# Kernel tuning notes

Hardware: AMD Instinct MI355X
Metric: run time of the kernel (lower is better)

Reference implementation:

```python
import jax, jax.numpy as jnp
import numpy as np

B, N, C = 4, 2048, 768
H = 12
D = C // H  # head_dim = 64
SCALE = D ** -0.5


def setup_inputs() -> dict:
    key = jax.random.key(0)
    ks = jax.random.split(key, 9)
    x = jax.random.normal(ks[0], (B, N, C), dtype=jnp.float32)
    k_in = jax.random.normal(ks[1], (B, N, C), dtype=jnp.float32)
    v_in = jax.random.normal(ks[2], (B, N, C), dtype=jnp.float32)
    rel_pos_bias = jax.random.normal(ks[3], (H, N, N), dtype=jnp.float32)
    # learned params (nn.Linear stores weight [out, in]; y = x @ W.T + b)
    s = C ** -0.5
    Wq = jax.random.normal(ks[4], (C, C), dtype=jnp.float32) * s
    Wk = jax.random.normal(ks[5], (C, C), dtype=jnp.float32) * s
    Wv = jax.random.normal(ks[6], (C, C), dtype=jnp.float32) * s
    Wp = jax.random.normal(ks[7], (C, C), dtype=jnp.float32) * s
    bp = jax.random.normal(ks[8], (C,), dtype=jnp.float32) * 0.01
    return {"x": x, "k_in": k_in, "v_in": v_in, "rel_pos_bias": rel_pos_bias,
            "Wq": Wq, "Wk": Wk, "Wv": Wv, "Wp": Wp, "bp": bp}


def reference(x, k_in, v_in, rel_pos_bias, Wq, Wk, Wv, Wp, bp):
    # linear projections (no q/k/v bias since qkv_bias=False)
    q = jnp.einsum('bnc,dc->bnd', x, Wq)      # [B,N,C]
    k = jnp.einsum('bnc,dc->bnd', k_in, Wk)   # [B,Nk,C]
    v = jnp.einsum('bnc,dc->bnd', v_in, Wv)   # [B,Nv,C]
    # split heads -> [B,H,N,D]
    q = q.reshape(B, N, H, D).transpose(0, 2, 1, 3) * SCALE
    k = k.reshape(B, -1, H, D).transpose(0, 2, 1, 3)
    v = v.reshape(B, -1, H, D).transpose(0, 2, 1, 3)
    attn = jnp.einsum('bhnd,bhmd->bhnm', q, k)          # [B,H,N,Nk]
    attn = attn + rel_pos_bias[None]                    # additive rel-pos bias
    attn = jax.nn.softmax(attn, axis=-1)
    out = jnp.einsum('bhnm,bhmd->bhnd', attn, v)        # [B,H,N,D]
    out = out.transpose(0, 2, 1, 3).reshape(B, N, C)
    return jnp.einsum('bnc,dc->bnd', out, Wp) + bp
```

## Files before the change

kernel.cpp:

```cpp
#include <hip/hip_runtime.h>
#include <stdint.h>
#include <stddef.h>

#define B_ 4
#define N_ 2048
#define C_ 768
#define H_ 12
#define M_ (B_ * N_)

typedef __attribute__((ext_vector_type(8))) short bf16x8_t;
typedef __attribute__((ext_vector_type(4))) float f32x4_t;

__device__ __forceinline__ unsigned pack2_bf16(float f0, float f1) {
  unsigned u0 = __builtin_bit_cast(unsigned, f0) + 0x8000u;
  unsigned u1 = __builtin_bit_cast(unsigned, f1) + 0x8000u;
  return __builtin_amdgcn_perm(u1, u0, 0x07060302u);
}

__device__ __forceinline__ short f2bf(float f) {
  unsigned u = __builtin_bit_cast(unsigned, f);
  u = (u + 0x7FFFu + ((u >> 16) & 1u)) >> 16;
  return (short)u;
}
__device__ __forceinline__ short f2bf_fast(float f) {
  return (short)((__builtin_bit_cast(unsigned, f) + 0x8000u) >> 16);
}

__device__ __forceinline__ void gload_lds16(const short* g, const short* l) {
  __builtin_amdgcn_global_load_lds(
      (const __attribute__((address_space(1))) void*)g,
      (__attribute__((address_space(3))) void*)l, 16, 0, 0);
}

#define XV 1572864
#define WV 147456
__global__ __launch_bounds__(256) void cvt_all(
    const float* __restrict__ x, const float* __restrict__ kin, const float* __restrict__ vin,
    const float* __restrict__ wq, const float* __restrict__ wk, const float* __restrict__ wv,
    const float* __restrict__ wp,
    unsigned short* __restrict__ xb, unsigned short* __restrict__ kb, unsigned short* __restrict__ vb,
    unsigned short* __restrict__ wqb, unsigned short* __restrict__ wkb, unsigned short* __restrict__ wvb,
    unsigned short* __restrict__ wpb)
{
  int i = blockIdx.x * 256 + threadIdx.x;
  const float* s; unsigned short* d; int off;
  if      (i < XV)            { s = x;   d = xb;  off = i; }
  else if (i < 2 * XV)        { s = kin; d = kb;  off = i - XV; }
  else if (i < 3 * XV)        { s = vin; d = vb;  off = i - 2 * XV; }
  else if (i < 3 * XV + WV)   { s = wq;  d = wqb; off = i - 3 * XV; }
  else if (i < 3 * XV + 2*WV) { s = wk;  d = wkb; off = i - 3 * XV - WV; }
  else if (i < 3 * XV + 3*WV) { s = wv;  d = wvb; off = i - 3 * XV - 2 * WV; }
  else                        { s = wp;  d = wpb; off = i - 3 * XV - 3 * WV; }
  float4 v = ((const float4*)s)[off];
  uint2 p;
  p.x = pack2_bf16(v.x, v.y);
  p.y = pack2_bf16(v.z, v.w);
  ((uint2*)d)[off] = p;
}

__global__ __launch_bounds__(256) void proj_qkv(
    const short* __restrict__ xb, const short* __restrict__ kb, const short* __restrict__ vb,
    const short* __restrict__ wqb, const short* __restrict__ wkb, const short* __restrict__ wvb,
    short* __restrict__ q_ws, short* __restrict__ k_ws, short* __restrict__ vt_ws)
{
  const int z = blockIdx.z;
  const short* A = (z == 0) ? xb : (z == 1) ? kb : vb;
  const short* W = (z == 0) ? wqb : (z == 1) ? wkb : wvb;
  const int m0 = blockIdx.x * 128;
  const int n0 = blockIdx.y * 128;

  __shared__ short As[128 * 64];
  __shared__ short Bs[128 * 64];

  const int t = threadIdx.x;
  const int w = t >> 6, L = t & 63, L15 = L & 15, quad = L >> 4;
  const int wm = w & 1, wn = w >> 1;

  f32x4_t acc[4][4] = {};

  const short* ga = A + (size_t)(m0 + w * 32 + (L >> 3)) * C_ + (L & 7) * 8;
  const short* gb = W + (size_t)(n0 + w * 32 + (L >> 3)) * C_ + (L & 7) * 8;
  const short* la = &As[(w * 32) * 64];
  const short* lb = &Bs[(w * 32) * 64];

  for (int k0 = 0; k0 < C_; k0 += 64) {
    __syncthreads();
    #pragma unroll
    for (int i = 0; i < 4; ++i) {
      gload_lds16(ga + (size_t)i * 8 * C_ + k0, la + i * 512);
      gload_lds16(gb + (size_t)i * 8 * C_ + k0, lb + i * 512);
    }
    __syncthreads();
    #pragma unroll
    for (int kk = 0; kk < 2; ++kk) {
      bf16x8_t af[4], bf[4];
      #pragma unroll
      for (int mt = 0; mt < 4; ++mt)
        af[mt] = *(const bf16x8_t*)&As[(wm * 64 + mt * 16 + L15) * 64 + kk * 32 + quad * 8];
      #pragma unroll
      for (int nt = 0; nt < 4; ++nt)
        bf[nt] = *(const bf16x8_t*)&Bs[(wn * 64 + nt * 16 + L15) * 64 + kk * 32 + quad * 8];
      #pragma unroll
      for (int mt = 0; mt < 4; ++mt)
        #pragma unroll
        for (int nt = 0; nt < 4; ++nt)
          acc[mt][nt] = __builtin_amdgcn_mfma_f32_16x16x32_bf16(af[mt], bf[nt], acc[mt][nt], 0, 0, 0);
    }
  }

  short* outp = (z == 0) ? q_ws : (z == 1) ? k_ws : vt_ws;
  const float mul = (z == 0) ? 0.125f : 1.0f;
  #pragma unroll
  for (int mt = 0; mt < 4; ++mt) {
    const int m_base = m0 + wm * 64 + mt * 16 + quad * 4;
    #pragma unroll
    for (int nt = 0; nt < 4; ++nt) {
      const int c = n0 + wn * 64 + nt * 16 + L15;
      const int h = c >> 6, d = c & 63;
      #pragma unroll
      for (int r = 0; r < 4; ++r) {
        const int m = m_base + r;
        const int b = m >> 11, n = m & 2047;
        const float v = acc[mt][nt][r] * mul;
        size_t idx;
        if (z == 2) idx = ((size_t)(b * H_ + h) * 64 + d) * N_ + n;
        else        idx = ((size_t)(b * H_ + h) * N_ + n) * 64 + d;
        outp[idx] = f2bf(v);
      }
    }
  }
}

__global__ __launch_bounds__(256) void attn(
    const short* __restrict__ q_ws, const short* __restrict__ k_ws,
    const short* __restrict__ vt_ws, const float* __restrict__ rpb,
    short* __restrict__ attn_out)
{
  const int b = blockIdx.x & 3;
  const int m0 = (blockIdx.x >> 2) * 64;
  const int h = blockIdx.y;
  const int bh = b * H_ + h;

  __shared__ short Qs[64][72];
  __shared__ short Ks[64][72];
  __shared__ short Vts[80][72];
  __shared__ short Ps[4][16][72];

  const int t = threadIdx.x;
  const int w = t >> 6, L = t & 63, L15 = L & 15, quad = L >> 4;
  const int sr = t >> 2, sc = (t & 3) << 4;

  const short* qp  = q_ws  + ((size_t)bh * N_ + m0) * 64;
  const short* kp  = k_ws  + (size_t)bh * N_ * 64;
  const short* vtp = vt_ws + (size_t)bh * 64 * N_;
  const float* bpb = rpb + (size_t)h * N_ * N_;

  {
    const short* g = qp + t * 16;
    *(uint4*)&Qs[sr][sc]     = *(const uint4*)g;
    *(uint4*)&Qs[sr][sc + 8] = *(const uint4*)(g + 8);
  }
  for (int i = t; i < 16 * 72; i += 256) {
    const int rr = i / 72, cc = i % 72;
    Vts[64 + rr][cc] = (rr == 0) ? (short)0x3F80 : (short)0;
  }

  f32x4_t o[5] = {};

  for (int kv0 = 0; kv0 < N_; kv0 += 64) {
    __syncthreads();
    {
      const short* gk = kp + (size_t)kv0 * 64 + t * 16;
      *(uint4*)&Ks[sr][sc]     = *(const uint4*)gk;
      *(uint4*)&Ks[sr][sc + 8] = *(const uint4*)(gk + 8);
      const short* gv = vtp + (size_t)sr * N_ + kv0 + sc;
      *(uint4*)&Vts[sr][sc]     = *(const uint4*)gv;
      *(uint4*)&Vts[sr][sc + 8] = *(const uint4*)(gv + 8);
    }
    float bias[4][4];
    {
      const float* bq = bpb + (size_t)(m0 + w * 16 + quad * 4) * N_ + kv0 + L15;
      #pragma unroll
      for (int r = 0; r < 4; ++r)
        #pragma unroll
        for (int nt = 0; nt < 4; ++nt)
          bias[r][nt] = bq[(size_t)r * N_ + nt * 16];
    }
    __syncthreads();

    bf16x8_t a0 = *(const bf16x8_t*)&Qs[w * 16 + L15][quad * 8];
    bf16x8_t a1 = *(const bf16x8_t*)&Qs[w * 16 + L15][32 + quad * 8];
    f32x4_t s[4];
    #pragma unroll
    for (int nt = 0; nt < 4; ++nt) {
      f32x4_t sv = {bias[0][nt], bias[1][nt], bias[2][nt], bias[3][nt]};
      bf16x8_t b0 = *(const bf16x8_t*)&Ks[nt * 16 + L15][quad * 8];
      bf16x8_t b1 = *(const bf16x8_t*)&Ks[nt * 16 + L15][32 + quad * 8];
      sv = __builtin_amdgcn_mfma_f32_16x16x32_bf16(a0, b0, sv, 0, 0, 0);
      s[nt] = __builtin_amdgcn_mfma_f32_16x16x32_bf16(a1, b1, sv, 0, 0, 0);
    }

    #pragma unroll
    for (int nt = 0; nt < 4; ++nt)
      #pragma unroll
      for (int r = 0; r < 4; ++r)
        Ps[w][quad * 4 + r][nt * 16 + L15] = f2bf_fast(__expf(s[nt][r]));

    #pragma unroll
    for (int kk = 0; kk < 2; ++kk) {
      bf16x8_t pa = *(const bf16x8_t*)&Ps[w][L15][kk * 32 + quad * 8];
      #pragma unroll
      for (int nt = 0; nt < 5; ++nt) {
        bf16x8_t vb = *(const bf16x8_t*)&Vts[nt * 16 + L15][kk * 32 + quad * 8];
        o[nt] = __builtin_amdgcn_mfma_f32_16x16x32_bf16(pa, vb, o[nt], 0, 0, 0);
      }
    }
  }

  float rl[4];
  #pragma unroll
  for (int r = 0; r < 4; ++r) {
    const float l = __shfl(o[4][r], quad * 16);
    rl[r] = 1.0f / l;
  }
  const int n_base = m0 + w * 16 + quad * 4;
  #pragma unroll
  for (int nt = 0; nt < 4; ++nt) {
    #pragma unroll
    for (int r = 0; r < 4; ++r) {
      const float v = o[nt][r] * rl[r];
      attn_out[((size_t)(b * N_ + n_base + r)) * C_ + h * 64 + nt * 16 + L15] = f2bf(v);
    }
  }
}

__global__ __launch_bounds__(256) void proj_out(
    const short* __restrict__ Abf, const short* __restrict__ wpb,
    const float* __restrict__ bpv, float* __restrict__ out)
{
  const int m0 = blockIdx.x * 128;
  const int n0 = blockIdx.y * 128;

  __shared__ short As[128 * 64];
  __shared__ short Bs[128 * 64];

  const int t = threadIdx.x;
  const int w = t >> 6, L = t & 63, L15 = L & 15, quad = L >> 4;
  const int wm = w & 1, wn = w >> 1;

  f32x4_t acc[4][4] = {};

  const short* ga = Abf + (size_t)(m0 + w * 32 + (L >> 3)) * C_ + (L & 7) * 8;
  const short* gb = wpb + (size_t)(n0 + w * 32 + (L >> 3)) * C_ + (L & 7) * 8;
  const short* la = &As[(w * 32) * 64];
  const short* lb = &Bs[(w * 32) * 64];

  for (int k0 = 0; k0 < C_; k0 += 64) {
    __syncthreads();
    #pragma unroll
    for (int i = 0; i < 4; ++i) {
      gload_lds16(ga + (size_t)i * 8 * C_ + k0, la + i * 512);
      gload_lds16(gb + (size_t)i * 8 * C_ + k0, lb + i * 512);
    }
    __syncthreads();
    #pragma unroll
    for (int kk = 0; kk < 2; ++kk) {
      bf16x8_t af[4], bf[4];
      #pragma unroll
      for (int mt = 0; mt < 4; ++mt)
        af[mt] = *(const bf16x8_t*)&As[(wm * 64 + mt * 16 + L15) * 64 + kk * 32 + quad * 8];
      #pragma unroll
      for (int nt = 0; nt < 4; ++nt)
        bf[nt] = *(const bf16x8_t*)&Bs[(wn * 64 + nt * 16 + L15) * 64 + kk * 32 + quad * 8];
      #pragma unroll
      for (int mt = 0; mt < 4; ++mt)
        #pragma unroll
        for (int nt = 0; nt < 4; ++nt)
          acc[mt][nt] = __builtin_amdgcn_mfma_f32_16x16x32_bf16(af[mt], bf[nt], acc[mt][nt], 0, 0, 0);
    }
  }

  #pragma unroll
  for (int mt = 0; mt < 4; ++mt) {
    const int m_base = m0 + wm * 64 + mt * 16 + quad * 4;
    #pragma unroll
    for (int nt = 0; nt < 4; ++nt) {
      const int c = n0 + wn * 64 + nt * 16 + L15;
      const float bb = bpv[c];
      #pragma unroll
      for (int r = 0; r < 4; ++r)
        out[(size_t)(m_base + r) * C_ + c] = acc[mt][nt][r] + bb;
    }
  }
}

extern "C" void kernel_launch(void* const* d_in, const int* in_sizes, int n_in,
                              void* d_out, int out_size, void* d_ws, size_t ws_size,
                              hipStream_t stream) {
  const float* x    = (const float*)d_in[0];
  const float* k_in = (const float*)d_in[1];
  const float* v_in = (const float*)d_in[2];
  const float* rpb  = (const float*)d_in[3];
  const float* Wq   = (const float*)d_in[4];
  const float* Wk   = (const float*)d_in[5];
  const float* Wv   = (const float*)d_in[6];
  const float* Wp   = (const float*)d_in[7];
  const float* bp   = (const float*)d_in[8];
  float* out = (float*)d_out;

  const size_t SZ = (size_t)B_ * H_ * N_ * 64 * sizeof(short);
  const size_t WSZ = (size_t)C_ * C_ * sizeof(short);
  char* ws = (char*)d_ws;
  short* q_ws  = (short*)(ws);
  short* k_ws  = (short*)(ws + SZ);
  short* vt_ws = (short*)(ws + 2 * SZ);
  short* ao_ws = (short*)(ws + 3 * SZ);
  short* xb    = (short*)(ws + 4 * SZ);
  short* kb    = (short*)(ws + 5 * SZ);
  short* vb    = (short*)(ws + 6 * SZ);
  short* wqb   = (short*)(ws + 7 * SZ);
  short* wkb   = (short*)(ws + 7 * SZ + WSZ);
  short* wvb   = (short*)(ws + 7 * SZ + 2 * WSZ);
  short* wpb   = (short*)(ws + 7 * SZ + 3 * WSZ);

  cvt_all<<<(3 * XV + 4 * WV + 255) / 256, 256, 0, stream>>>(
      x, k_in, v_in, Wq, Wk, Wv, Wp,
      (unsigned short*)xb, (unsigned short*)kb, (unsigned short*)vb,
      (unsigned short*)wqb, (unsigned short*)wkb, (unsigned short*)wvb, (unsigned short*)wpb);
  proj_qkv<<<dim3(M_ / 128, C_ / 128, 3), 256, 0, stream>>>(
      xb, kb, vb, wqb, wkb, wvb, q_ws, k_ws, vt_ws);
  attn<<<dim3(B_ * (N_ / 64), H_), 256, 0, stream>>>(q_ws, k_ws, vt_ws, rpb, ao_ws);
  proj_out<<<dim3(M_ / 128, C_ / 128), 256, 0, stream>>>(ao_ws, wpb, bp, out);
}
```

Baseline: 512.2 us.

## Stage QKV epilogue through LDS and use direct global-to-LDS loads in attention

The QKV projection epilogue now writes bf16 results into shared memory, transposed for V, and then emits coalesced 16-byte global stores instead of scattered 2-byte stores. The attention kernel replaces register-staged Q/K/V^T loads with gload_lds16 direct-to-LDS copies into unpadded 64-wide tiles. The cost is two extra barriers and a larger LDS footprint in the projection kernel. The unpadded Q/K/V tiles may also cause LDS bank conflicts on the MFMA operand reads.

After: 532.5 us. 1.04x slower.

```diff
diff --git a/kernel.cpp b/kernel.cpp
--- a/kernel.cpp
+++ b/kernel.cpp
@@ -69,8 +69,9 @@
   const int m0 = blockIdx.x * 128;
   const int n0 = blockIdx.y * 128;
 
-  __shared__ short As[128 * 64];
-  __shared__ short Bs[128 * 64];
+  __shared__ short smem[128 * 136];
+  short* As = smem;
+  short* Bs = smem + 8192;
 
   const int t = threadIdx.x;
   const int w = t >> 6, L = t & 63, L15 = L & 15, quad = L >> 4;
@@ -93,41 +94,62 @@
     __syncthreads();
     #pragma unroll
     for (int kk = 0; kk < 2; ++kk) {
-      bf16x8_t af[4], bf[4];
+      bf16x8_t af[4], bfr[4];
       #pragma unroll
       for (int mt = 0; mt < 4; ++mt)
         af[mt] = *(const bf16x8_t*)&As[(wm * 64 + mt * 16 + L15) * 64 + kk * 32 + quad * 8];
       #pragma unroll
       for (int nt = 0; nt < 4; ++nt)
-        bf[nt] = *(const bf16x8_t*)&Bs[(wn * 64 + nt * 16 + L15) * 64 + kk * 32 + quad * 8];
+        bfr[nt] = *(const bf16x8_t*)&Bs[(wn * 64 + nt * 16 + L15) * 64 + kk * 32 + quad * 8];
       #pragma unroll
       for (int mt = 0; mt < 4; ++mt)
         #pragma unroll
         for (int nt = 0; nt < 4; ++nt)
-          acc[mt][nt] = __builtin_amdgcn_mfma_f32_16x16x32_bf16(af[mt], bf[nt], acc[mt][nt], 0, 0, 0);
-    }
-  }
+          acc[mt][nt] = __builtin_amdgcn_mfma_f32_16x16x32_bf16(af[mt], bfr[nt], acc[mt][nt], 0, 0, 0);
+    }
+  }
+
+  __syncthreads();
+  if (z != 2) {
+    const float mul = (z == 0) ? 0.125f : 1.0f;
+    #pragma unroll
+    for (int mt = 0; mt < 4; ++mt)
+      #pragma unroll
+      for (int nt = 0; nt < 4; ++nt)
+        #pragma unroll
+        for (int r = 0; r < 4; ++r)
+          smem[(wm * 64 + mt * 16 + quad * 4 + r) * 136 + wn * 64 + nt * 16 + L15] =
+              f2bf(acc[mt][nt][r] * mul);
+  } else {
+    #pragma unroll
+    for (int nt = 0; nt < 4; ++nt)
+      #pragma unroll
+      for (int mt = 0; mt < 4; ++mt) {
+        uint2 p;
+        p.x = pack2_bf16(acc[mt][nt][0], acc[mt][nt][1]);
+        p.y = pack2_bf16(acc[mt][nt][2], acc[mt][nt][3]);
+        *(uint2*)&smem[(wn * 64 + nt * 16 + L15) * 136 + wm * 64 + mt * 16 + quad * 4] = p;
+      }
+  }
+  __syncthreads();
 
   short* outp = (z == 0) ? q_ws : (z == 1) ? k_ws : vt_ws;
-  const float mul = (z == 0) ? 0.125f : 1.0f;
-  #pragma unroll
-  for (int mt = 0; mt < 4; ++mt) {
-    const int m_base = m0 + wm * 64 + mt * 16 + quad * 4;
-    #pragma unroll
-    for (int nt = 0; nt < 4; ++nt) {
-      const int c = n0 + wn * 64 + nt * 16 + L15;
-      const int h = c >> 6, d = c & 63;
-      #pragma unroll
-      for (int r = 0; r < 4; ++r) {
-        const int m = m_base + r;
-        const int b = m >> 11, n = m & 2047;
-        const float v = acc[mt][nt][r] * mul;
-        size_t idx;
-        if (z == 2) idx = ((size_t)(b * H_ + h) * 64 + d) * N_ + n;
-        else        idx = ((size_t)(b * H_ + h) * N_ + n) * 64 + d;
-        outp[idx] = f2bf(v);
-      }
-    }
+  const int b = m0 >> 11, nb = m0 & 2047;
+  #pragma unroll
+  for (int it = 0; it < 8; ++it) {
+    const int run = w * 64 + it * 8 + (L >> 3);
+    const int row = run >> 1, half = run & 1;
+    uint4 val = *(const uint4*)&smem[row * 136 + half * 64 + (L & 7) * 8];
+    size_t g;
+    if (z != 2) {
+      const int h = (n0 >> 6) + half;
+      const int m = m0 + row;
+      g = (((size_t)((m >> 11) * H_ + h) * N_ + (m & 2047))) * 64 + (L & 7) * 8;
+    } else {
+      const int c = n0 + row, h = c >> 6, d = c & 63;
+      g = ((size_t)(b * H_ + h) * 64 + d) * N_ + nb + half * 64 + (L & 7) * 8;
+    }
+    *(uint4*)(outp + g) = val;
   }
 }
 
@@ -141,41 +163,36 @@
   const int h = blockIdx.y;
   const int bh = b * H_ + h;
 
-  __shared__ short Qs[64][72];
-  __shared__ short Ks[64][72];
-  __shared__ short Vts[80][72];
-  __shared__ short Ps[4][16][72];
+  __shared__ short Qs[64 * 64];
+  __shared__ short Ks[64 * 64];
+  __shared__ short Vts[80 * 64];
+  __shared__ short Ps[4][16 * 72];
 
   const int t = threadIdx.x;
   const int w = t >> 6, L = t & 63, L15 = L & 15, quad = L >> 4;
-  const int sr = t >> 2, sc = (t & 3) << 4;
 
   const short* qp  = q_ws  + ((size_t)bh * N_ + m0) * 64;
   const short* kp  = k_ws  + (size_t)bh * N_ * 64;
   const short* vtp = vt_ws + (size_t)bh * 64 * N_;
   const float* bpb = rpb + (size_t)h * N_ * N_;
 
-  {
-    const short* g = qp + t * 16;
-    *(uint4*)&Qs[sr][sc]     = *(const uint4*)g;
-    *(uint4*)&Qs[sr][sc + 8] = *(const uint4*)(g + 8);
-  }
-  for (int i = t; i < 16 * 72; i += 256) {
-    const int rr = i / 72, cc = i % 72;
-    Vts[64 + rr][cc] = (rr == 0) ? (short)0x3F80 : (short)0;
-  }
+  #pragma unroll
+  for (int i = 0; i < 2; ++i) {
+    const int r0 = w * 16 + i * 8;
+    gload_lds16(qp + r0 * 64 + L * 8, &Qs[r0 * 64]);
+  }
+  for (int i = t; i < 16 * 64; i += 256)
+    Vts[64 * 64 + i] = (i < 64) ? (short)0x3F80 : (short)0;
 
   f32x4_t o[5] = {};
 
   for (int kv0 = 0; kv0 < N_; kv0 += 64) {
     __syncthreads();
-    {
-      const short* gk = kp + (size_t)kv0 * 64 + t * 16;
-      *(uint4*)&Ks[sr][sc]     = *(const uint4*)gk;
-      *(uint4*)&Ks[sr][sc + 8] = *(const uint4*)(gk + 8);
-      const short* gv = vtp + (size_t)sr * N_ + kv0 + sc;
-      *(uint4*)&Vts[sr][sc]     = *(const uint4*)gv;
-      *(uint4*)&Vts[sr][sc + 8] = *(const uint4*)(gv + 8);
+    #pragma unroll
+    for (int i = 0; i < 2; ++i) {
+      const int r0 = w * 16 + i * 8;
+      gload_lds16(kp + (size_t)(kv0 + r0) * 64 + L * 8, &Ks[r0 * 64]);
+      gload_lds16(vtp + (size_t)(r0 + (L >> 3)) * N_ + kv0 + (L & 7) * 8, &Vts[r0 * 64]);
     }
     float bias[4][4];
     {
@@ -188,14 +205,14 @@
     }
     __syncthreads();
 
-    bf16x8_t a0 = *(const bf16x8_t*)&Qs[w * 16 + L15][quad * 8];
-    bf16x8_t a1 = *(const bf16x8_t*)&Qs[w * 16 + L15][32 + quad * 8];
+    bf16x8_t a0 = *(const bf16x8_t*)&Qs[(w * 16 + L15) * 64 + quad * 8];
+    bf16x8_t a1 = *(const bf16x8_t*)&Qs[(w * 16 + L15) * 64 + 32 + quad * 8];
     f32x4_t s[4];
     #pragma unroll
     for (int nt = 0; nt < 4; ++nt) {
       f32x4_t sv = {bias[0][nt], bias[1][nt], bias[2][nt], bias[3][nt]};
-      bf16x8_t b0 = *(const bf16x8_t*)&Ks[nt * 16 + L15][quad * 8];
-      bf16x8_t b1 = *(const bf16x8_t*)&Ks[nt * 16 + L15][32 + quad * 8];
+      bf16x8_t b0 = *(const bf16x8_t*)&Ks[(nt * 16 + L15) * 64 + quad * 8];
+      bf16x8_t b1 = *(const bf16x8_t*)&Ks[(nt * 16 + L15) * 64 + 32 + quad * 8];
       sv = __builtin_amdgcn_mfma_f32_16x16x32_bf16(a0, b0, sv, 0, 0, 0);
       s[nt] = __builtin_amdgcn_mfma_f32_16x16x32_bf16(a1, b1, sv, 0, 0, 0);
     }
@@ -204,14 +221,14 @@
     for (int nt = 0; nt < 4; ++nt)
       #pragma unroll
       for (int r = 0; r < 4; ++r)
-        Ps[w][quad * 4 + r][nt * 16 + L15] = f2bf_fast(__expf(s[nt][r]));
+        Ps[w][(quad * 4 + r) * 72 + nt * 16 + L15] = f2bf_fast(__expf(s[nt][r]));
 
     #pragma unroll
     for (int kk = 0; kk < 2; ++kk) {
-      bf16x8_t pa = *(const bf16x8_t*)&Ps[w][L15][kk * 32 + quad * 8];
+      bf16x8_t pa = *(const bf16x8_t*)&Ps[w][L15 * 72 + kk * 32 + quad * 8];
       #pragma unroll
       for (int nt = 0; nt < 5; ++nt) {
-        bf16x8_t vb = *(const bf16x8_t*)&Vts[nt * 16 + L15][kk * 32 + quad * 8];
+        bf16x8_t vb = *(const bf16x8_t*)&Vts[(nt * 16 + L15) * 64 + kk * 32 + quad * 8];
         o[nt] = __builtin_amdgcn_mfma_f32_16x16x32_bf16(pa, vb, o[nt], 0, 0, 0);
       }
     }
@@ -265,18 +282,18 @@
     __syncthreads();
     #pragma unroll
     for (int kk = 0; kk < 2; ++kk) {
-      bf16x8_t af[4], bf[4];
+      bf16x8_t af[4], bfr[4];
       #pragma unroll
       for (int mt = 0; mt < 4; ++mt)
         af[mt] = *(const bf16x8_t*)&As[(wm * 64 + mt * 16 + L15) * 64 + kk * 32 + quad * 8];
       #pragma unroll
       for (int nt = 0; nt < 4; ++nt)
-        bf[nt] = *(const bf16x8_t*)&Bs[(wn * 64 + nt * 16 + L15) * 64 + kk * 32 + quad * 8];
+        bfr[nt] = *(const bf16x8_t*)&Bs[(wn * 64 + nt * 16 + L15) * 64 + kk * 32 + quad * 8];
       #pragma unroll
       for (int mt = 0; mt < 4; ++mt)
         #pragma unroll
         for (int nt = 0; nt < 4; ++nt)
-          acc[mt][nt] = __builtin_amdgcn_mfma_f32_16x16x32_bf16(af[mt], bf[nt], acc[mt][nt], 0, 0, 0);
+          acc[mt][nt] = __builtin_amdgcn_mfma_f32_16x16x32_bf16(af[mt], bfr[nt], acc[mt][nt], 0, 0, 0);
     }
   }
 
```
